# Optimization experiments

Measured on AMD Instinct MI355X. Metric: run time of the kernel, lower is better.

Reference implementation:

```python
import jax, jax.numpy as jnp
import numpy as np
from jax import lax

RADII = (0.1, 0.2, 0.4)
NBRS = (16, 32, 64)
PE_DIM = 24
CENTER_PE_DIM = 96
EPS = 1e-5


def sinusoidal_3d(x, dim):
    # x: [..., 3] -> [..., dim]; dim//3 features per axis (half sin, half cos)
    per_axis = dim // 3
    half = per_axis // 2
    freq = jnp.exp(-jnp.log(10000.0) * jnp.arange(half, dtype=x.dtype) / (half - 1))
    ang = x[..., None] * freq                      # [..., 3, half]
    emb = jnp.concatenate([jnp.sin(ang), jnp.cos(ang)], axis=-1)  # [..., 3, per_axis]
    return emb.reshape(x.shape[:-1] + (dim,))


def layer_norm(x, g, b):
    m = jnp.mean(x, axis=-1, keepdims=True)
    v = jnp.var(x, axis=-1, keepdims=True)
    return (x - m) * lax.rsqrt(v + EPS) * g + b


def point_mlp(x, W, b, g, beta, act):
    y = layer_norm(x @ W + b, g, beta)
    return jax.nn.gelu(y, approximate=False) if act else y


def index_points(pts, idx):
    # pts: [B,N,C], idx: [B,...] -> [B,...,C]
    bidx = jnp.arange(pts.shape[0]).reshape((-1,) + (1,) * (idx.ndim - 1))
    return pts[bidx, idx]


def farthest_point_sample(xyz, npoint):
    # xyz: [B,N,3] -> idx [B,npoint]
    N = xyz.shape[1]

    def single(pts):
        def step(carry, _):
            dist, far = carry
            c = pts[far]                                   # [3]
            d = jnp.sum((pts - c) ** 2, axis=-1)           # [N]
            dist = jnp.minimum(dist, d)
            nxt = jnp.argmax(dist).astype(jnp.int32)
            return (dist, nxt), far
        init = (jnp.full((N,), 1e10, pts.dtype), jnp.int32(0))
        _, idxs = lax.scan(step, init, None, length=npoint)
        return idxs

    return jax.vmap(single)(xyz)


def query_ball_point(radius, k, xyz, centers):
    # xyz: [B,N,3], centers: [B,S,3] -> [B,S,k] neighbor indices
    N = xyz.shape[1]
    sqr = jnp.sum((centers[:, :, None, :] - xyz[:, None, :, :]) ** 2, axis=-1)  # [B,S,N]
    gidx = jnp.where(sqr > radius * radius, N, jnp.arange(N)[None, None, :])
    gidx = jnp.sort(gidx, axis=-1)[..., :k]
    first = gidx[..., :1]
    return jnp.where(gidx == N, first, gidx)


def setup_inputs() -> dict:
    key = jax.random.key(0)
    ks = jax.random.split(key, 8)
    B, N, STEM, TOK = 16, 4096, 128, 256
    d_in = STEM + 3 + PE_DIM          # 155
    d_tok_in = STEM + 3 * TOK + CENTER_PE_DIM  # 992
    sc = 0.02
    return {
        "xyz": jax.random.uniform(ks[0], (B, N, 3), dtype=jnp.float32),
        "point_feature": jax.random.normal(ks[1], (B, N, STEM), dtype=jnp.float32) * 0.1,
        "sW1": jax.random.normal(ks[2], (3, d_in, TOK), dtype=jnp.float32) * sc,
        "sb1": jnp.zeros((3, TOK)), "sg1": jnp.ones((3, TOK)), "sbeta1": jnp.zeros((3, TOK)),
        "sW2": jax.random.normal(ks[3], (3, TOK, TOK), dtype=jnp.float32) * sc,
        "sb2": jnp.zeros((3, TOK)), "sg2": jnp.ones((3, TOK)), "sbeta2": jnp.zeros((3, TOK)),
        "tW1": jax.random.normal(ks[4], (d_tok_in, TOK), dtype=jnp.float32) * sc,
        "tb1": jnp.zeros((TOK,)), "tg1": jnp.ones((TOK,)), "tbeta1": jnp.zeros((TOK,)),
        "tW2": jax.random.normal(ks[5], (TOK, TOK), dtype=jnp.float32) * sc,
        "tb2": jnp.zeros((TOK,)), "tg2": jnp.ones((TOK,)), "tbeta2": jnp.zeros((TOK,)),
    }


def reference(xyz, point_feature, sW1, sb1, sg1, sbeta1, sW2, sb2, sg2, sbeta2,
              tW1, tb1, tg1, tbeta1, tW2, tb2, tg2, tbeta2):
    S = 512  # num_patches
    center_idx = farthest_point_sample(xyz, S)            # [B,S]
    patch_center = index_points(xyz, center_idx)          # [B,S,3]
    center_feature = index_points(point_feature, center_idx)  # [B,S,STEM]

    scale_feats = []
    for s, (r, k) in enumerate(zip(RADII, NBRS)):
        nidx = query_ball_point(r, k, xyz, patch_center)  # [B,S,k]
        gxyz = index_points(xyz, nidx)                    # [B,S,k,3]
        gfeat = index_points(point_feature, nidx)         # [B,S,k,STEM]
        rel = gxyz - patch_center[:, :, None, :]
        rel_pe = sinusoidal_3d(rel, PE_DIM)
        gin = jnp.concatenate([gfeat, rel, rel_pe], axis=-1)   # [B,S,k,155]
        h = point_mlp(gin, sW1[s], sb1[s], sg1[s], sbeta1[s], True)
        h = point_mlp(h, sW2[s], sb2[s], sg2[s], sbeta2[s], False)
        scale_feats.append(jnp.max(h, axis=2))            # [B,S,TOK]

    center_pe = sinusoidal_3d(patch_center, CENTER_PE_DIM)    # [B,S,96]
    tok_in = jnp.concatenate([center_feature] + scale_feats + [center_pe], axis=-1)
    tok = point_mlp(tok_in, tW1, tb1, tg1, tbeta1, True)
    tok = point_mlp(tok, tW2, tb2, tg2, tbeta2, False)
    return tok, patch_center
```

## Files before the change

kernel.cpp:

```cpp
#include <hip/hip_runtime.h>
#include <math.h>

#define BATCH 16
#define NPTS  4096
#define NCTR  512
#define STEM  128
#define TOK   256
#define D_IN  155
#define D_TOK 992

typedef short s16x8 __attribute__((ext_vector_type(8)));
typedef float f32x4 __attribute__((ext_vector_type(4)));

static constexpr float FR15c[16] = {
    1.0f, 0.5411695265464638f, 0.2928644487857941f, 0.15848931670188904f,
    0.08576958626508713f, 0.04641588851809502f, 0.02511886507272720f, 0.01359356392547488f,
    0.007356422487646341f, 0.003981071710586548f, 0.002154434798285365f, 0.001165914465673268f,
    0.0006309573450125754f, 0.0003414548910222948f, 0.0001847849769866168f, 0.0001f};

__device__ __forceinline__ unsigned short f2bf(float f) {
    unsigned u = __float_as_uint(f);
    u += 0x7FFF + ((u >> 16) & 1);
    return (unsigned short)(u >> 16);
}
__device__ __forceinline__ float bf2f(unsigned short b) {
    return __uint_as_float(((unsigned)b) << 16);
}

__device__ __forceinline__ void bsplit8(const float* v, s16x8& hi, s16x8& lo) {
    union { s16x8 s; unsigned w[4]; } H, L;
#pragma unroll
    for (int p = 0; p < 4; ++p) {
        unsigned hp, lp;
        asm("v_cvt_pk_bf16_f32 %0, %1, %2" : "=v"(hp) : "v"(v[2 * p]), "v"(v[2 * p + 1]));
        float r0 = v[2 * p]     - __uint_as_float(hp << 16);
        float r1 = v[2 * p + 1] - __uint_as_float(hp & 0xffff0000u);
        asm("v_cvt_pk_bf16_f32 %0, %1, %2" : "=v"(lp) : "v"(r0), "v"(r1));
        H.w[p] = hp; L.w[p] = lp;
    }
    hi = H.s; lo = L.s;
}

__device__ __forceinline__ void pkpair(float v0, float v1, unsigned& w0, unsigned& w1) {
    unsigned hp, lp;
    asm("v_cvt_pk_bf16_f32 %0, %1, %2" : "=v"(hp) : "v"(v0), "v"(v1));
    float r0 = v0 - __uint_as_float(hp << 16);
    float r1 = v1 - __uint_as_float(hp & 0xffff0000u);
    asm("v_cvt_pk_bf16_f32 %0, %1, %2" : "=v"(lp) : "v"(r0), "v"(r1));
    w0 = (hp << 16) | (lp & 0xffffu);
    w1 = (hp & 0xffff0000u) | (lp >> 16);
}

__device__ __forceinline__ void loadB(const unsigned short* __restrict__ pk,
                                      int frag, int l, s16x8& bh, s16x8& bl) {
    const unsigned short* p = pk + (size_t)frag * 1024 + (size_t)l * 8;
    bh = *(const s16x8*)p;
    bl = *(const s16x8*)(p + 512);
}

__device__ __forceinline__ float gelu_exact(float x) {
    float z = x * 0.70710678118654752f;
    float a = fabsf(z);
    float t = __builtin_amdgcn_rcpf(fmaf(0.3275911f, a, 1.0f));
    float p = fmaf(1.061405429f, t, -1.453152027f);
    p = fmaf(p, t, 1.421413741f);
    p = fmaf(p, t, -0.284496736f);
    p = fmaf(p, t, 0.254829592f);
    p = p * t;
    float e = __expf(-z * z);
    float y = fmaf(-p, e, 1.0f);
    y = (z < 0.0f) ? -y : y;
    return 0.5f * x * (1.0f + y);
}

__device__ __forceinline__ float sq3(float ax, float ay, float az,
                                     float bx, float by, float bz) {
    float dx = __fsub_rn(ax, bx);
    float dy = __fsub_rn(ay, by);
    float dz = __fsub_rn(az, bz);
    float d = __fmul_rn(dx, dx);
    d = __fadd_rn(d, __fmul_rn(dy, dy));
    d = __fadd_rn(d, __fmul_rn(dz, dz));
    return d;
}

__global__ __launch_bounds__(256) void fps_kernel(const float* __restrict__ xyz,
                                                  int* __restrict__ center_idx,
                                                  float* __restrict__ pc_ws,
                                                  float* __restrict__ pc_out) {
    int b = blockIdx.x;
    int t = threadIdx.x;
    const int w = t >> 6, lane = t & 63;
    const float* X = xyz + (size_t)b * NPTS * 3;
    __shared__ __align__(16) float sxyz[NPTS * 3];
    __shared__ float swv[2][4];
    __shared__ int   swi[2][4];
    __shared__ int   hist[NCTR];
    {
        const float4* src = (const float4*)X;
        float4* dst = (float4*)sxyz;
        for (int i = t; i < NPTS * 3 / 4; i += 256) dst[i] = src[i];
    }
    __syncthreads();
    float px[16], py[16], pz[16], dist[16];
#pragma unroll
    for (int j = 0; j < 16; ++j) {
        int i = t + 256 * j;
        px[j] = sxyz[i * 3 + 0];
        py[j] = sxyz[i * 3 + 1];
        pz[j] = sxyz[i * 3 + 2];
        dist[j] = 1e10f;
    }
    int far = 0;
    for (int s = 0; s < NCTR; ++s) {
        if (t == 0) hist[s] = far;
        float cx = sxyz[far * 3 + 0];
        float cy = sxyz[far * 3 + 1];
        float cz = sxyz[far * 3 + 2];
        float bv = -1.0f;
        int bi = 0;
#pragma unroll
        for (int j = 0; j < 16; ++j) {
            float d = sq3(px[j], py[j], pz[j], cx, cy, cz);
            float nd = fminf(dist[j], d);
            dist[j] = nd;
            if (nd > bv) { bv = nd; bi = t + 256 * j; }
        }
#pragma unroll
        for (int off = 32; off >= 1; off >>= 1) {
            float ov = __shfl_xor(bv, off, 64);
            int   oi = __shfl_xor(bi, off, 64);
            if (ov > bv || (ov == bv && oi < bi)) { bv = ov; bi = oi; }
        }
        const int p = s & 1;
        if (lane == 0) { swv[p][w] = bv; swi[p][w] = bi; }
        __syncthreads();
        bv = swv[p][0]; bi = swi[p][0];
#pragma unroll
        for (int ww = 1; ww < 4; ++ww) {
            float ov = swv[p][ww]; int oi = swi[p][ww];
            if (ov > bv || (ov == bv && oi < bi)) { bv = ov; bi = oi; }
        }
        far = bi;
    }
    __syncthreads();
    for (int s = t; s < NCTR; s += 256) {
        int idx = hist[s];
        center_idx[b * NCTR + s] = idx;
        float cx = sxyz[idx * 3], cy = sxyz[idx * 3 + 1], cz = sxyz[idx * 3 + 2];
        size_t po = (size_t)(b * NCTR + s) * 3;
        pc_ws[po] = cx; pc_ws[po + 1] = cy; pc_ws[po + 2] = cz;
        pc_out[po] = cx; pc_out[po + 1] = cy; pc_out[po + 2] = cz;
    }
}

template <int K>
__global__ __launch_bounds__(256) void ballq_kernel(const float* __restrict__ xyz,
                                                    const float* __restrict__ pc,
                                                    int* __restrict__ nbr,
                                                    float rr) {
    int cid = blockIdx.x * 4 + (threadIdx.x >> 6);
    int lane = threadIdx.x & 63;
    int b = cid >> 9;
    const float* X = xyz + (size_t)b * NPTS * 3;
    float cx = pc[(size_t)cid * 3 + 0];
    float cy = pc[(size_t)cid * 3 + 1];
    float cz = pc[(size_t)cid * 3 + 2];
    int cnt = 0, first = 0;
    bool have_first = false;
    long long base = (long long)cid * K;
    for (int it = 0; it < NPTS / 64; ++it) {
        int i = it * 64 + lane;
        float d = sq3(cx, cy, cz, X[i * 3], X[i * 3 + 1], X[i * 3 + 2]);
        bool ok = d <= rr;
        unsigned long long mask = __ballot(ok);
        if (!have_first && mask) {
            first = it * 64 + (int)__builtin_ctzll(mask);
            have_first = true;
        }
        int pos = cnt + (int)__popcll(mask & ((1ull << lane) - 1ull));
        if (ok && pos < K) nbr[base + pos] = i;
        cnt += (int)__popcll(mask);
        if (cnt >= K) break;
    }
    int fill = cnt < K ? cnt : K;
    for (int j = fill + lane; j < K; j += 64) nbr[base + j] = first;
}

__global__ __launch_bounds__(256) void pack_w(const float* __restrict__ Wbase,
                                              unsigned short* __restrict__ out,
                                              int Kdim, int KS) {
    int s = blockIdx.y;
    const float* W = Wbase + (size_t)s * Kdim * TOK;
    unsigned short* o = out + (size_t)s * 16 * KS * 64 * 16;
    int tid = blockIdx.x * 256 + threadIdx.x;
    if (tid >= 16 * KS * 64) return;
    int lane = tid & 63;
    int frag = tid >> 6;
    int ks = frag % KS;
    int ct = frag / KS;
    int col = ct * 16 + (lane & 15);
    int k0 = ks * 32 + (lane >> 4) * 8;
    unsigned short* hi = o + (size_t)frag * 1024 + lane * 8;
    unsigned short* lo = hi + 512;
#pragma unroll
    for (int j = 0; j < 8; ++j) {
        int k = k0 + j;
        float v = (k < Kdim) ? W[(size_t)k * TOK + col] : 0.0f;
        unsigned short h = f2bf(v);
        hi[j] = h;
        lo[j] = f2bf(v - bf2f(h));
    }
}

template <int K>
__global__ __launch_bounds__(256, 2) void scale_mfma(
    const float* __restrict__ xyz, const float* __restrict__ pf,
    const unsigned short* __restrict__ pk1, const float* __restrict__ b1,
    const float* __restrict__ g1, const float* __restrict__ be1,
    const unsigned short* __restrict__ pk2, const float* __restrict__ b2,
    const float* __restrict__ g2, const float* __restrict__ be2,
    const int* __restrict__ nbr, const float* __restrict__ pc,
    float* __restrict__ outf) {
    __shared__ unsigned int hpk[64][260];
    __shared__ float lnred[4][64][2];
    const int w = threadIdx.x >> 6, l = threadIdx.x & 63;
    const int lg = l >> 4, li = l & 15;
    const int ws4 = 4 * w;

    int nb[4];
    float relx[4], rely[4], relz[4];
#pragma unroll
    for (int rb = 0; rb < 4; ++rb) {
        int row_g = blockIdx.x * 64 + rb * 16 + li;
        int c = (blockIdx.x * 64 + rb * 16) / K;
        int b = c >> 9;
        int n = nbr[row_g];
        nb[rb] = b * NPTS + n;
        const float* X = xyz + (size_t)nb[rb] * 3;
        const float* C = pc + (size_t)c * 3;
        relx[rb] = __fsub_rn(X[0], C[0]);
        rely[rb] = __fsub_rn(X[1], C[1]);
        relz[rb] = __fsub_rn(X[2], C[2]);
    }

    f32x4 acc1[4][4];
#pragma unroll
    for (int rb = 0; rb < 4; ++rb)
#pragma unroll
        for (int ctl = 0; ctl < 4; ++ctl) acc1[rb][ctl] = (f32x4){0.f, 0.f, 0.f, 0.f};

#pragma unroll
    for (int ks = 0; ks < 5; ++ks) {
        s16x8 Bh[4], Bl[4];
#pragma unroll
        for (int ctl = 0; ctl < 4; ++ctl)
            loadB(pk1, (ws4 + ctl) * 5 + ks, l, Bh[ctl], Bl[ctl]);
        s16x8 Ah[4], Al[4];
#pragma unroll
        for (int rb = 0; rb < 4; ++rb) {
            float v[8];
            if (ks < 4) {
                const float* src = pf + (size_t)nb[rb] * STEM + ks * 32 + lg * 8;
                float4 f0 = *(const float4*)src;
                float4 f1 = *(const float4*)(src + 4);
                v[0] = f0.x; v[1] = f0.y; v[2] = f0.z; v[3] = f0.w;
                v[4] = f1.x; v[5] = f1.y; v[6] = f1.z; v[7] = f1.w;
            } else {
#pragma unroll
                for (int j = 0; j < 8; ++j) {
                    int ch = lg * 8 + j;
                    float val = 0.0f;
                    if (ch < 3) {
                        val = (ch == 0) ? relx[rb] : ((ch == 1) ? rely[rb] : relz[rb]);
                    } else if (ch < 27) {
                        int rem = ch - 3;
                        int axis = rem >> 3, r8 = rem & 7;
                        int fi = (r8 < 4) ? r8 : r8 - 4;
                        float fr = (fi == 0) ? 1.0f
                                  : (fi == 1) ? 0.046415888336127795f
                                  : (fi == 2) ? 0.0021544346900318843f : 1e-4f;
                        float rl = (axis == 0) ? relx[rb] : ((axis == 1) ? rely[rb] : relz[rb]);
                        float ang = rl * fr;
                        val = (r8 < 4) ? __sinf(ang) : __cosf(ang);
                    }
                    v[j] = val;
                }
            }
            bsplit8(v, Ah[rb], Al[rb]);
        }
#pragma unroll
        for (int ctl = 0; ctl < 4; ++ctl)
#pragma unroll
            for (int rb = 0; rb < 4; ++rb) {
                acc1[rb][ctl] = __builtin_amdgcn_mfma_f32_16x16x32_bf16(Ah[rb], Bh[ctl], acc1[rb][ctl], 0, 0, 0);
                acc1[rb][ctl] = __builtin_amdgcn_mfma_f32_16x16x32_bf16(Ah[rb], Bl[ctl], acc1[rb][ctl], 0, 0, 0);
                acc1[rb][ctl] = __builtin_amdgcn_mfma_f32_16x16x32_bf16(Al[rb], Bh[ctl], acc1[rb][ctl], 0, 0, 0);
            }
    }

    {
        float b1v[4], g1v[4], be1v[4];
#pragma unroll
        for (int ctl = 0; ctl < 4; ++ctl) {
            int col = w * 64 + ctl * 16 + li;
            b1v[ctl] = b1[col]; g1v[ctl] = g1[col]; be1v[ctl] = be1[col];
        }
#pragma unroll
        for (int rb = 0; rb < 4; ++rb)
#pragma unroll
            for (int reg = 0; reg < 4; ++reg) {
                float s = 0.f, ss = 0.f;
#pragma unroll
                for (int ctl = 0; ctl < 4; ++ctl) {
                    float x = acc1[rb][ctl][reg] + b1v[ctl];
                    s += x; ss = fmaf(x, x, ss);
                }
#pragma unroll
                for (int m = 1; m <= 8; m <<= 1) {
                    s += __shfl_xor(s, m, 64);
                    ss += __shfl_xor(ss, m, 64);
                }
                if (li == 0) {
                    lnred[w][rb * 16 + lg * 4 + reg][0] = s;
                    lnred[w][rb * 16 + lg * 4 + reg][1] = ss;
                }
            }
        __syncthreads();
#pragma unroll
        for (int rb = 0; rb < 4; ++rb)
#pragma unroll
            for (int reg = 0; reg < 4; ++reg) {
                int row = rb * 16 + lg * 4 + reg;
                float s = lnred[0][row][0] + lnred[1][row][0] + lnred[2][row][0] + lnred[3][row][0];
                float ss = lnred[0][row][1] + lnred[1][row][1] + lnred[2][row][1] + lnred[3][row][1];
                float mean = s * (1.0f / 256.0f);
                float var = ss * (1.0f / 256.0f) - mean * mean;
                float rs = rsqrtf(var + 1e-5f);
#pragma unroll
                for (int ctl = 0; ctl < 4; ++ctl) {
                    float x = acc1[rb][ctl][reg] + b1v[ctl];
                    acc1[rb][ctl][reg] = gelu_exact((x - mean) * rs * g1v[ctl] + be1v[ctl]);
                }
            }
    }

#pragma unroll
    for (int rb = 0; rb < 4; ++rb)
#pragma unroll
        for (int ctl = 0; ctl < 4; ++ctl) {
            unsigned w0, w1, w2, w3;
            pkpair(acc1[rb][ctl][0], acc1[rb][ctl][1], w0, w1);
            pkpair(acc1[rb][ctl][2], acc1[rb][ctl][3], w2, w3);
            int r0 = rb * 16 + lg * 4;
            int kc = w * 64 + ctl * 16 + li;
            hpk[r0 + 0][kc] = w0; hpk[r0 + 1][kc] = w1;
            hpk[r0 + 2][kc] = w2; hpk[r0 + 3][kc] = w3;
        }
    __syncthreads();

    f32x4 acc2[4][4];
#pragma unroll
    for (int rb = 0; rb < 4; ++rb)
#pragma unroll
        for (int ctl = 0; ctl < 4; ++ctl) acc2[rb][ctl] = (f32x4){0.f, 0.f, 0.f, 0.f};

#pragma unroll
    for (int q = 0; q < 8; ++q) {
        s16x8 Bh[4], Bl[4];
#pragma unroll
        for (int ctl = 0; ctl < 4; ++ctl)
            loadB(pk2, (ws4 + ctl) * 8 + q, l, Bh[ctl], Bl[ctl]);
#pragma unroll
        for (int rb = 0; rb < 4; ++rb) {
            const unsigned int* hp = &hpk[rb * 16 + li][q * 32 + lg * 8];
            int4 xa = *(const int4*)hp;
            int4 xb = *(const int4*)(hp + 4);
            unsigned x[8] = {(unsigned)xa.x, (unsigned)xa.y, (unsigned)xa.z, (unsigned)xa.w,
                             (unsigned)xb.x, (unsigned)xb.y, (unsigned)xb.z, (unsigned)xb.w};
            union { s16x8 s; unsigned w[4]; } H, L;
#pragma unroll
            for (int p = 0; p < 4; ++p) {
                H.w[p] = (x[2 * p] >> 16) | (x[2 * p + 1] & 0xffff0000u);
                L.w[p] = (x[2 * p] & 0xffffu) | (x[2 * p + 1] << 16);
            }
#pragma unroll
            for (int ctl = 0; ctl < 4; ++ctl) {
                acc2[rb][ctl] = __builtin_amdgcn_mfma_f32_16x16x32_bf16(H.s, Bh[ctl], acc2[rb][ctl], 0, 0, 0);
                acc2[rb][ctl] = __builtin_amdgcn_mfma_f32_16x16x32_bf16(H.s, Bl[ctl], acc2[rb][ctl], 0, 0, 0);
                acc2[rb][ctl] = __builtin_amdgcn_mfma_f32_16x16x32_bf16(L.s, Bh[ctl], acc2[rb][ctl], 0, 0, 0);
            }
        }
    }

    float b2v[4], g2v[4], be2v[4];
#pragma unroll
    for (int ctl = 0; ctl < 4; ++ctl) {
        int col = w * 64 + ctl * 16 + li;
        b2v[ctl] = b2[col]; g2v[ctl] = g2[col]; be2v[ctl] = be2[col];
    }
#pragma unroll
    for (int rb = 0; rb < 4; ++rb)
#pragma unroll
        for (int reg = 0; reg < 4; ++reg) {
            float s = 0.f, ss = 0.f;
#pragma unroll
            for (int ctl = 0; ctl < 4; ++ctl) {
                float x = acc2[rb][ctl][reg] + b2v[ctl];
                s += x; ss = fmaf(x, x, ss);
            }
#pragma unroll
            for (int m = 1; m <= 8; m <<= 1) {
                s += __shfl_xor(s, m, 64);
                ss += __shfl_xor(ss, m, 64);
            }
            if (li == 0) {
                lnred[w][rb * 16 + lg * 4 + reg][0] = s;
                lnred[w][rb * 16 + lg * 4 + reg][1] = ss;
            }
        }
    __syncthreads();
#pragma unroll
    for (int rb = 0; rb < 4; ++rb)
#pragma unroll
        for (int reg = 0; reg < 4; ++reg) {
            int row = rb * 16 + lg * 4 + reg;
            float s = lnred[0][row][0] + lnred[1][row][0] + lnred[2][row][0] + lnred[3][row][0];
            float ss = lnred[0][row][1] + lnred[1][row][1] + lnred[2][row][1] + lnred[3][row][1];
            float mean = s * (1.0f / 256.0f);
            float var = ss * (1.0f / 256.0f) - mean * mean;
            float rs = rsqrtf(var + 1e-5f);
#pragma unroll
            for (int ctl = 0; ctl < 4; ++ctl) {
                float x = acc2[rb][ctl][reg] + b2v[ctl];
                acc2[rb][ctl][reg] = (x - mean) * rs * g2v[ctl] + be2v[ctl];
            }
        }

    const int CPB = 64 / K;
    const int RBC = K / 16;
#pragma unroll
    for (int cg = 0; cg < CPB; ++cg)
#pragma unroll
        for (int ctl = 0; ctl < 4; ++ctl) {
            float mx = -3.4e38f;
#pragma unroll
            for (int rbl = 0; rbl < RBC; ++rbl) {
                int rb = cg * RBC + rbl;
#pragma unroll
                for (int reg = 0; reg < 4; ++reg) mx = fmaxf(mx, acc2[rb][ctl][reg]);
            }
            mx = fmaxf(mx, __shfl_xor(mx, 16, 64));
            mx = fmaxf(mx, __shfl_xor(mx, 32, 64));
            if (lg == 0)
                outf[(size_t)(blockIdx.x * CPB + cg) * TOK + w * 64 + ctl * 16 + li] = mx;
        }
}

__global__ __launch_bounds__(256, 2) void token_mfma(
    const float* __restrict__ pf, const int* __restrict__ center_idx,
    const float* __restrict__ pc, const float* __restrict__ sf0,
    const float* __restrict__ sf1, const float* __restrict__ sf2,
    const unsigned short* __restrict__ pk1, const float* __restrict__ b1,
    const float* __restrict__ g1, const float* __restrict__ be1,
    const unsigned short* __restrict__ pk2, const float* __restrict__ b2,
    const float* __restrict__ g2, const float* __restrict__ be2,
    float* __restrict__ out) {
    __shared__ unsigned int hpk[32][260];
    __shared__ float lnred[4][32][2];
    const int w = threadIdx.x >> 6, l = threadIdx.x & 63;
    const int lg = l >> 4, li = l & 15;
    const int ws4 = 4 * w;
    const int rowbase = blockIdx.x * 32;

    int rowg[2];
    const float* pfc[2];
    float pcx[2], pcy[2], pcz[2];
#pragma unroll
    for (int rb = 0; rb < 2; ++rb) {
        int row = rowbase + rb * 16 + li;
        rowg[rb] = row;
        int b = row >> 9;
        int cidx = center_idx[row];
        pfc[rb] = pf + ((size_t)b * NPTS + cidx) * STEM;
        pcx[rb] = pc[(size_t)row * 3 + 0];
        pcy[rb] = pc[(size_t)row * 3 + 1];
        pcz[rb] = pc[(size_t)row * 3 + 2];
    }

    f32x4 acc1[2][4];
#pragma unroll
    for (int rb = 0; rb < 2; ++rb)
#pragma unroll
        for (int ctl = 0; ctl < 4; ++ctl) acc1[rb][ctl] = (f32x4){0.f, 0.f, 0.f, 0.f};

#pragma unroll 2
    for (int ks = 0; ks < 31; ++ks) {
        s16x8 Bh[4], Bl[4];
#pragma unroll
        for (int ctl = 0; ctl < 4; ++ctl)
            loadB(pk1, (ws4 + ctl) * 31 + ks, l, Bh[ctl], Bl[ctl]);
        s16x8 Ah[2], Al[2];
#pragma unroll
        for (int rb = 0; rb < 2; ++rb) {
            float v[8];
            if (ks < 28) {
                const float* src;
                if (ks < 4)       src = pfc[rb] + ks * 32 + lg * 8;
                else if (ks < 12) src = sf0 + (size_t)rowg[rb] * TOK + (ks - 4) * 32 + lg * 8;
                else if (ks < 20) src = sf1 + (size_t)rowg[rb] * TOK + (ks - 12) * 32 + lg * 8;
                else              src = sf2 + (size_t)rowg[rb] * TOK + (ks - 20) * 32 + lg * 8;
                float4 f0 = *(const float4*)src;
                float4 f1 = *(const float4*)(src + 4);
                v[0] = f0.x; v[1] = f0.y; v[2] = f0.z; v[3] = f0.w;
                v[4] = f1.x; v[5] = f1.y; v[6] = f1.z; v[7] = f1.w;
            } else {
                float c = (ks == 28) ? pcx[rb] : ((ks == 29) ? pcy[rb] : pcz[rb]);
#pragma unroll
                for (int j = 0; j < 8; ++j) {
                    float fr = (lg & 1) ? FR15c[8 + j] : FR15c[j];
                    float ang = c * fr;
                    v[j] = (lg < 2) ? __sinf(ang) : __cosf(ang);
                }
            }
            bsplit8(v, Ah[rb], Al[rb]);
        }
#pragma unroll
        for (int ctl = 0; ctl < 4; ++ctl)
#pragma unroll
            for (int rb = 0; rb < 2; ++rb) {
                acc1[rb][ctl] = __builtin_amdgcn_mfma_f32_16x16x32_bf16(Ah[rb], Bh[ctl], acc1[rb][ctl], 0, 0, 0);
                acc1[rb][ctl] = __builtin_amdgcn_mfma_f32_16x16x32_bf16(Ah[rb], Bl[ctl], acc1[rb][ctl], 0, 0, 0);
                acc1[rb][ctl] = __builtin_amdgcn_mfma_f32_16x16x32_bf16(Al[rb], Bh[ctl], acc1[rb][ctl], 0, 0, 0);
            }
    }

    {
        float b1v[4], g1v[4], be1v[4];
#pragma unroll
        for (int ctl = 0; ctl < 4; ++ctl) {
            int col = w * 64 + ctl * 16 + li;
            b1v[ctl] = b1[col]; g1v[ctl] = g1[col]; be1v[ctl] = be1[col];
        }
#pragma unroll
        for (int rb = 0; rb < 2; ++rb)
#pragma unroll
            for (int reg = 0; reg < 4; ++reg) {
                float s = 0.f, ss = 0.f;
#pragma unroll
                for (int ctl = 0; ctl < 4; ++ctl) {
                    float x = acc1[rb][ctl][reg] + b1v[ctl];
                    s += x; ss = fmaf(x, x, ss);
                }
#pragma unroll
                for (int m = 1; m <= 8; m <<= 1) {
                    s += __shfl_xor(s, m, 64);
                    ss += __shfl_xor(ss, m, 64);
                }
                if (li == 0) {
                    lnred[w][rb * 16 + lg * 4 + reg][0] = s;
                    lnred[w][rb * 16 + lg * 4 + reg][1] = ss;
                }
            }
        __syncthreads();
#pragma unroll
        for (int rb = 0; rb < 2; ++rb)
#pragma unroll
            for (int reg = 0; reg < 4; ++reg) {
                int row = rb * 16 + lg * 4 + reg;
                float s = lnred[0][row][0] + lnred[1][row][0] + lnred[2][row][0] + lnred[3][row][0];
                float ss = lnred[0][row][1] + lnred[1][row][1] + lnred[2][row][1] + lnred[3][row][1];
                float mean = s * (1.0f / 256.0f);
                float var = ss * (1.0f / 256.0f) - mean * mean;
                float rs = rsqrtf(var + 1e-5f);
#pragma unroll
                for (int ctl = 0; ctl < 4; ++ctl) {
                    float x = acc1[rb][ctl][reg] + b1v[ctl];
                    acc1[rb][ctl][reg] = gelu_exact((x - mean) * rs * g1v[ctl] + be1v[ctl]);
                }
            }
    }

#pragma unroll
    for (int rb = 0; rb < 2; ++rb)
#pragma unroll
        for (int ctl = 0; ctl < 4; ++ctl) {
            unsigned w0, w1, w2, w3;
            pkpair(acc1[rb][ctl][0], acc1[rb][ctl][1], w0, w1);
            pkpair(acc1[rb][ctl][2], acc1[rb][ctl][3], w2, w3);
            int r0 = rb * 16 + lg * 4;
            int kc = w * 64 + ctl * 16 + li;
            hpk[r0 + 0][kc] = w0; hpk[r0 + 1][kc] = w1;
            hpk[r0 + 2][kc] = w2; hpk[r0 + 3][kc] = w3;
        }
    __syncthreads();

    f32x4 acc2[2][4];
#pragma unroll
    for (int rb = 0; rb < 2; ++rb)
#pragma unroll
        for (int ctl = 0; ctl < 4; ++ctl) acc2[rb][ctl] = (f32x4){0.f, 0.f, 0.f, 0.f};
#pragma unroll
    for (int q = 0; q < 8; ++q) {
        s16x8 Bh[4], Bl[4];
#pragma unroll
        for (int ctl = 0; ctl < 4; ++ctl)
            loadB(pk2, (ws4 + ctl) * 8 + q, l, Bh[ctl], Bl[ctl]);
#pragma unroll
        for (int rb = 0; rb < 2; ++rb) {
            const unsigned int* hp = &hpk[rb * 16 + li][q * 32 + lg * 8];
            int4 xa = *(const int4*)hp;
            int4 xb = *(const int4*)(hp + 4);
            unsigned x[8] = {(unsigned)xa.x, (unsigned)xa.y, (unsigned)xa.z, (unsigned)xa.w,
                             (unsigned)xb.x, (unsigned)xb.y, (unsigned)xb.z, (unsigned)xb.w};
            union { s16x8 s; unsigned w[4]; } H, L;
#pragma unroll
            for (int p = 0; p < 4; ++p) {
                H.w[p] = (x[2 * p] >> 16) | (x[2 * p + 1] & 0xffff0000u);
                L.w[p] = (x[2 * p] & 0xffffu) | (x[2 * p + 1] << 16);
            }
#pragma unroll
            for (int ctl = 0; ctl < 4; ++ctl) {
                acc2[rb][ctl] = __builtin_amdgcn_mfma_f32_16x16x32_bf16(H.s, Bh[ctl], acc2[rb][ctl], 0, 0, 0);
                acc2[rb][ctl] = __builtin_amdgcn_mfma_f32_16x16x32_bf16(H.s, Bl[ctl], acc2[rb][ctl], 0, 0, 0);
                acc2[rb][ctl] = __builtin_amdgcn_mfma_f32_16x16x32_bf16(L.s, Bh[ctl], acc2[rb][ctl], 0, 0, 0);
            }
        }
    }

    float b2v[4], g2v[4], be2v[4];
#pragma unroll
    for (int ctl = 0; ctl < 4; ++ctl) {
        int col = w * 64 + ctl * 16 + li;
        b2v[ctl] = b2[col]; g2v[ctl] = g2[col]; be2v[ctl] = be2[col];
    }
#pragma unroll
    for (int rb = 0; rb < 2; ++rb)
#pragma unroll
        for (int reg = 0; reg < 4; ++reg) {
            float s = 0.f, ss = 0.f;
#pragma unroll
            for (int ctl = 0; ctl < 4; ++ctl) {
                float x = acc2[rb][ctl][reg] + b2v[ctl];
                s += x; ss = fmaf(x, x, ss);
            }
#pragma unroll
            for (int m = 1; m <= 8; m <<= 1) {
                s += __shfl_xor(s, m, 64);
                ss += __shfl_xor(ss, m, 64);
            }
            if (li == 0) {
                lnred[w][rb * 16 + lg * 4 + reg][0] = s;
                lnred[w][rb * 16 + lg * 4 + reg][1] = ss;
            }
        }
    __syncthreads();
#pragma unroll
    for (int rb = 0; rb < 2; ++rb)
#pragma unroll
        for (int reg = 0; reg < 4; ++reg) {
            int row = rb * 16 + lg * 4 + reg;
            float s = lnred[0][row][0] + lnred[1][row][0] + lnred[2][row][0] + lnred[3][row][0];
            float ss = lnred[0][row][1] + lnred[1][row][1] + lnred[2][row][1] + lnred[3][row][1];
            float mean = s * (1.0f / 256.0f);
            float var = ss * (1.0f / 256.0f) - mean * mean;
            float rs = rsqrtf(var + 1e-5f);
#pragma unroll
            for (int ctl = 0; ctl < 4; ++ctl) {
                float x = acc2[rb][ctl][reg] + b2v[ctl];
                float v = (x - mean) * rs * g2v[ctl] + be2v[ctl];
                out[(size_t)(rowbase + row) * TOK + w * 64 + ctl * 16 + li] = v;
            }
        }
}

extern "C" void kernel_launch(void* const* d_in, const int* in_sizes, int n_in,
                              void* d_out, int out_size, void* d_ws, size_t ws_size,
                              hipStream_t stream) {
    const float* xyz  = (const float*)d_in[0];
    const float* pf   = (const float*)d_in[1];
    const float* sW1  = (const float*)d_in[2];
    const float* sb1  = (const float*)d_in[3];
    const float* sg1  = (const float*)d_in[4];
    const float* sbe1 = (const float*)d_in[5];
    const float* sW2  = (const float*)d_in[6];
    const float* sb2  = (const float*)d_in[7];
    const float* sg2  = (const float*)d_in[8];
    const float* sbe2 = (const float*)d_in[9];
    const float* tW1  = (const float*)d_in[10];
    const float* tb1  = (const float*)d_in[11];
    const float* tg1  = (const float*)d_in[12];
    const float* tbe1 = (const float*)d_in[13];
    const float* tW2  = (const float*)d_in[14];
    const float* tb2  = (const float*)d_in[15];
    const float* tg2  = (const float*)d_in[16];
    const float* tbe2 = (const float*)d_in[17];

    float* out_tok = (float*)d_out;
    float* out_pc  = out_tok + (size_t)BATCH * NCTR * TOK;

    char* ws = (char*)d_ws;
    int* center_idx = (int*)ws;   ws += (size_t)BATCH * NCTR * 4;
    float* pc_ws    = (float*)ws; ws += (size_t)BATCH * NCTR * 3 * 4;
    int* nbr0       = (int*)ws;   ws += (size_t)BATCH * NCTR * 16 * 4;
    int* nbr1       = (int*)ws;   ws += (size_t)BATCH * NCTR * 32 * 4;
    int* nbr2       = (int*)ws;   ws += (size_t)BATCH * NCTR * 64 * 4;
    float* sf0      = (float*)ws; ws += (size_t)BATCH * NCTR * TOK * 4;
    float* sf1      = (float*)ws; ws += (size_t)BATCH * NCTR * TOK * 4;
    float* sf2      = (float*)ws; ws += (size_t)BATCH * NCTR * TOK * 4;
    const size_t PK1_S  = 16 * 5 * 64 * 16;
    const size_t PK2_S  = 16 * 8 * 64 * 16;
    const size_t PKT1_S = 16 * 31 * 64 * 16;
    const size_t PKT2_S = 16 * 8 * 64 * 16;
    unsigned short* pkW1 = (unsigned short*)ws; ws += 3 * PK1_S * 2;
    unsigned short* pkW2 = (unsigned short*)ws; ws += 3 * PK2_S * 2;
    unsigned short* pkT1 = (unsigned short*)ws; ws += PKT1_S * 2;
    unsigned short* pkT2 = (unsigned short*)ws; ws += PKT2_S * 2;

    {
        dim3 gp1((16 * 5 * 64 + 255) / 256, 3);
        pack_w<<<gp1, 256, 0, stream>>>(sW1, pkW1, D_IN, 5);
        dim3 gp2((16 * 8 * 64 + 255) / 256, 3);
        pack_w<<<gp2, 256, 0, stream>>>(sW2, pkW2, TOK, 8);
        dim3 gpt1((16 * 31 * 64 + 255) / 256, 1);
        pack_w<<<gpt1, 256, 0, stream>>>(tW1, pkT1, D_TOK, 31);
        dim3 gpt2((16 * 8 * 64 + 255) / 256, 1);
        pack_w<<<gpt2, 256, 0, stream>>>(tW2, pkT2, TOK, 8);
    }

    fps_kernel<<<BATCH, 256, 0, stream>>>(xyz, center_idx, pc_ws, out_pc);

    ballq_kernel<16><<<BATCH * NCTR / 4, 256, 0, stream>>>(xyz, pc_ws, nbr0, (float)(0.1 * 0.1));
    ballq_kernel<32><<<BATCH * NCTR / 4, 256, 0, stream>>>(xyz, pc_ws, nbr1, (float)(0.2 * 0.2));
    ballq_kernel<64><<<BATCH * NCTR / 4, 256, 0, stream>>>(xyz, pc_ws, nbr2, (float)(0.4 * 0.4));

    scale_mfma<16><<<(BATCH * NCTR * 16) / 64, 256, 0, stream>>>(
        xyz, pf, pkW1 + 0 * PK1_S, sb1 + 0 * TOK, sg1 + 0 * TOK, sbe1 + 0 * TOK,
        pkW2 + 0 * PK2_S, sb2 + 0 * TOK, sg2 + 0 * TOK, sbe2 + 0 * TOK,
        nbr0, pc_ws, sf0);
    scale_mfma<32><<<(BATCH * NCTR * 32) / 64, 256, 0, stream>>>(
        xyz, pf, pkW1 + 1 * PK1_S, sb1 + 1 * TOK, sg1 + 1 * TOK, sbe1 + 1 * TOK,
        pkW2 + 1 * PK2_S, sb2 + 1 * TOK, sg2 + 1 * TOK, sbe2 + 1 * TOK,
        nbr1, pc_ws, sf1);
    scale_mfma<64><<<(BATCH * NCTR * 64) / 64, 256, 0, stream>>>(
        xyz, pf, pkW1 + 2 * PK1_S, sb1 + 2 * TOK, sg1 + 2 * TOK, sbe1 + 2 * TOK,
        pkW2 + 2 * PK2_S, sb2 + 2 * TOK, sg2 + 2 * TOK, sbe2 + 2 * TOK,
        nbr2, pc_ws, sf2);

    token_mfma<<<(BATCH * NCTR) / 32, 256, 0, stream>>>(
        pf, center_idx, pc_ws, sf0, sf1, sf2,
        pkT1, tb1, tg1, tbe1, pkT2, tb2, tg2, tbe2, out_tok);
}
```

Baseline: 1.634 ms.

## Halve scale MLP block tile to 32 rows and defer K=64 max to token kernel

Each scale_mfma block now handles 32 neighbor rows instead of 64, which halves accumulator registers and LDS use and doubles the grid. This is meant to raise occupancy or cut register pressure and spills. With K=64 a center now spans two blocks, so those blocks write partial maxima to a doubled buffer. token_mfma takes the max of the two partials while loading its input. The cost is more blocks, more reloads of the packed weights, and extra global traffic for the K=64 partials.

```diff
diff --git a/kernel.cpp b/kernel.cpp
--- a/kernel.cpp
+++ b/kernel.cpp
@@ -222,18 +222,18 @@
     const float* __restrict__ g2, const float* __restrict__ be2,
     const int* __restrict__ nbr, const float* __restrict__ pc,
     float* __restrict__ outf) {
-    __shared__ unsigned int hpk[64][260];
-    __shared__ float lnred[4][64][2];
+    __shared__ unsigned int hpk[32][260];
+    __shared__ float lnred[4][32][2];
     const int w = threadIdx.x >> 6, l = threadIdx.x & 63;
     const int lg = l >> 4, li = l & 15;
     const int ws4 = 4 * w;
 
-    int nb[4];
-    float relx[4], rely[4], relz[4];
-#pragma unroll
-    for (int rb = 0; rb < 4; ++rb) {
-        int row_g = blockIdx.x * 64 + rb * 16 + li;
-        int c = (blockIdx.x * 64 + rb * 16) / K;
+    int nb[2];
+    float relx[2], rely[2], relz[2];
+#pragma unroll
+    for (int rb = 0; rb < 2; ++rb) {
+        int row_g = blockIdx.x * 32 + rb * 16 + li;
+        int c = (blockIdx.x * 32 + rb * 16) / K;
         int b = c >> 9;
         int n = nbr[row_g];
         nb[rb] = b * NPTS + n;
@@ -244,9 +244,9 @@
         relz[rb] = __fsub_rn(X[2], C[2]);
     }
 
-    f32x4 acc1[4][4];
-#pragma unroll
-    for (int rb = 0; rb < 4; ++rb)
+    f32x4 acc1[2][4];
+#pragma unroll
+    for (int rb = 0; rb < 2; ++rb)
 #pragma unroll
         for (int ctl = 0; ctl < 4; ++ctl) acc1[rb][ctl] = (f32x4){0.f, 0.f, 0.f, 0.f};
 
@@ -256,9 +256,9 @@
 #pragma unroll
         for (int ctl = 0; ctl < 4; ++ctl)
             loadB(pk1, (ws4 + ctl) * 5 + ks, l, Bh[ctl], Bl[ctl]);
-        s16x8 Ah[4], Al[4];
-#pragma unroll
-        for (int rb = 0; rb < 4; ++rb) {
+        s16x8 Ah[2], Al[2];
+#pragma unroll
+        for (int rb = 0; rb < 2; ++rb) {
             float v[8];
             if (ks < 4) {
                 const float* src = pf + (size_t)nb[rb] * STEM + ks * 32 + lg * 8;
@@ -292,7 +292,7 @@
 #pragma unroll
         for (int ctl = 0; ctl < 4; ++ctl)
 #pragma unroll
-            for (int rb = 0; rb < 4; ++rb) {
+            for (int rb = 0; rb < 2; ++rb) {
                 acc1[rb][ctl] = __builtin_amdgcn_mfma_f32_16x16x32_bf16(Ah[rb], Bh[ctl], acc1[rb][ctl], 0, 0, 0);
                 acc1[rb][ctl] = __builtin_amdgcn_mfma_f32_16x16x32_bf16(Ah[rb], Bl[ctl], acc1[rb][ctl], 0, 0, 0);
                 acc1[rb][ctl] = __builtin_amdgcn_mfma_f32_16x16x32_bf16(Al[rb], Bh[ctl], acc1[rb][ctl], 0, 0, 0);
@@ -307,7 +307,7 @@
             b1v[ctl] = b1[col]; g1v[ctl] = g1[col]; be1v[ctl] = be1[col];
         }
 #pragma unroll
-        for (int rb = 0; rb < 4; ++rb)
+        for (int rb = 0; rb < 2; ++rb)
 #pragma unroll
             for (int reg = 0; reg < 4; ++reg) {
                 float s = 0.f, ss = 0.f;
@@ -328,7 +328,7 @@
             }
         __syncthreads();
 #pragma unroll
-        for (int rb = 0; rb < 4; ++rb)
+        for (int rb = 0; rb < 2; ++rb)
 #pragma unroll
             for (int reg = 0; reg < 4; ++reg) {
                 int row = rb * 16 + lg * 4 + reg;
@@ -346,7 +346,7 @@
     }
 
 #pragma unroll
-    for (int rb = 0; rb < 4; ++rb)
+    for (int rb = 0; rb < 2; ++rb)
 #pragma unroll
         for (int ctl = 0; ctl < 4; ++ctl) {
             unsigned w0, w1, w2, w3;
@@ -359,9 +359,9 @@
         }
     __syncthreads();
 
-    f32x4 acc2[4][4];
-#pragma unroll
-    for (int rb = 0; rb < 4; ++rb)
+    f32x4 acc2[2][4];
+#pragma unroll
+    for (int rb = 0; rb < 2; ++rb)
 #pragma unroll
         for (int ctl = 0; ctl < 4; ++ctl) acc2[rb][ctl] = (f32x4){0.f, 0.f, 0.f, 0.f};
 
@@ -372,7 +372,7 @@
         for (int ctl = 0; ctl < 4; ++ctl)
             loadB(pk2, (ws4 + ctl) * 8 + q, l, Bh[ctl], Bl[ctl]);
 #pragma unroll
-        for (int rb = 0; rb < 4; ++rb) {
+        for (int rb = 0; rb < 2; ++rb) {
             const unsigned int* hp = &hpk[rb * 16 + li][q * 32 + lg * 8];
             int4 xa = *(const int4*)hp;
             int4 xb = *(const int4*)(hp + 4);
@@ -400,7 +400,7 @@
         b2v[ctl] = b2[col]; g2v[ctl] = g2[col]; be2v[ctl] = be2[col];
     }
 #pragma unroll
-    for (int rb = 0; rb < 4; ++rb)
+    for (int rb = 0; rb < 2; ++rb)
 #pragma unroll
         for (int reg = 0; reg < 4; ++reg) {
             float s = 0.f, ss = 0.f;
@@ -421,7 +421,7 @@
         }
     __syncthreads();
 #pragma unroll
-    for (int rb = 0; rb < 4; ++rb)
+    for (int rb = 0; rb < 2; ++rb)
 #pragma unroll
         for (int reg = 0; reg < 4; ++reg) {
             int row = rb * 16 + lg * 4 + reg;
@@ -437,30 +437,39 @@
             }
         }
 
-    const int CPB = 64 / K;
-    const int RBC = K / 16;
-#pragma unroll
-    for (int cg = 0; cg < CPB; ++cg)
+    if (K == 16) {
+#pragma unroll
+        for (int rb = 0; rb < 2; ++rb)
+#pragma unroll
+            for (int ctl = 0; ctl < 4; ++ctl) {
+                float mx = -3.4e38f;
+#pragma unroll
+                for (int reg = 0; reg < 4; ++reg) mx = fmaxf(mx, acc2[rb][ctl][reg]);
+                mx = fmaxf(mx, __shfl_xor(mx, 16, 64));
+                mx = fmaxf(mx, __shfl_xor(mx, 32, 64));
+                if (lg == 0)
+                    outf[(size_t)(blockIdx.x * 2 + rb) * TOK + w * 64 + ctl * 16 + li] = mx;
+            }
+    } else {
 #pragma unroll
         for (int ctl = 0; ctl < 4; ++ctl) {
             float mx = -3.4e38f;
 #pragma unroll
-            for (int rbl = 0; rbl < RBC; ++rbl) {
-                int rb = cg * RBC + rbl;
+            for (int rb = 0; rb < 2; ++rb)
 #pragma unroll
                 for (int reg = 0; reg < 4; ++reg) mx = fmaxf(mx, acc2[rb][ctl][reg]);
-            }
             mx = fmaxf(mx, __shfl_xor(mx, 16, 64));
             mx = fmaxf(mx, __shfl_xor(mx, 32, 64));
             if (lg == 0)
-                outf[(size_t)(blockIdx.x * CPB + cg) * TOK + w * 64 + ctl * 16 + li] = mx;
-        }
+                outf[(size_t)blockIdx.x * TOK + w * 64 + ctl * 16 + li] = mx;
+        }
+    }
 }
 
 __global__ __launch_bounds__(256, 2) void token_mfma(
     const float* __restrict__ pf, const int* __restrict__ center_idx,
     const float* __restrict__ pc, const float* __restrict__ sf0,
-    const float* __restrict__ sf1, const float* __restrict__ sf2,
+    const float* __restrict__ sf1, const float* __restrict__ sf2p,
     const unsigned short* __restrict__ pk1, const float* __restrict__ b1,
     const float* __restrict__ g1, const float* __restrict__ be1,
     const unsigned short* __restrict__ pk2, const float* __restrict__ b2,
@@ -504,16 +513,26 @@
 #pragma unroll
         for (int rb = 0; rb < 2; ++rb) {
             float v[8];
-            if (ks < 28) {
+            if (ks < 20) {
                 const float* src;
                 if (ks < 4)       src = pfc[rb] + ks * 32 + lg * 8;
                 else if (ks < 12) src = sf0 + (size_t)rowg[rb] * TOK + (ks - 4) * 32 + lg * 8;
-                else if (ks < 20) src = sf1 + (size_t)rowg[rb] * TOK + (ks - 12) * 32 + lg * 8;
-                else              src = sf2 + (size_t)rowg[rb] * TOK + (ks - 20) * 32 + lg * 8;
+                else              src = sf1 + (size_t)rowg[rb] * TOK + (ks - 12) * 32 + lg * 8;
                 float4 f0 = *(const float4*)src;
                 float4 f1 = *(const float4*)(src + 4);
                 v[0] = f0.x; v[1] = f0.y; v[2] = f0.z; v[3] = f0.w;
                 v[4] = f1.x; v[5] = f1.y; v[6] = f1.z; v[7] = f1.w;
+            } else if (ks < 28) {
+                const float* sa = sf2p + ((size_t)rowg[rb] * 2) * TOK + (ks - 20) * 32 + lg * 8;
+                const float* sb = sa + TOK;
+                float4 a0 = *(const float4*)sa;
+                float4 a1 = *(const float4*)(sa + 4);
+                float4 b0 = *(const float4*)sb;
+                float4 b1 = *(const float4*)(sb + 4);
+                v[0] = fmaxf(a0.x, b0.x); v[1] = fmaxf(a0.y, b0.y);
+                v[2] = fmaxf(a0.z, b0.z); v[3] = fmaxf(a0.w, b0.w);
+                v[4] = fmaxf(a1.x, b1.x); v[5] = fmaxf(a1.y, b1.y);
+                v[6] = fmaxf(a1.z, b1.z); v[7] = fmaxf(a1.w, b1.w);
             } else {
                 float c = (ks == 28) ? pcx[rb] : ((ks == 29) ? pcy[rb] : pcz[rb]);
 #pragma unroll
@@ -707,7 +726,7 @@
     int* nbr2       = (int*)ws;   ws += (size_t)BATCH * NCTR * 64 * 4;
     float* sf0      = (float*)ws; ws += (size_t)BATCH * NCTR * TOK * 4;
     float* sf1      = (float*)ws; ws += (size_t)BATCH * NCTR * TOK * 4;
-    float* sf2      = (float*)ws; ws += (size_t)BATCH * NCTR * TOK * 4;
+    float* sf2p     = (float*)ws; ws += (size_t)BATCH * NCTR * 2 * TOK * 4;
     const size_t PK1_S  = 16 * 5 * 64 * 16;
     const size_t PK2_S  = 16 * 8 * 64 * 16;
     const size_t PKT1_S = 16 * 31 * 64 * 16;
@@ -734,20 +753,20 @@
     ballq_kernel<32><<<BATCH * NCTR / 4, 256, 0, stream>>>(xyz, pc_ws, nbr1, (float)(0.2 * 0.2));
     ballq_kernel<64><<<BATCH * NCTR / 4, 256, 0, stream>>>(xyz, pc_ws, nbr2, (float)(0.4 * 0.4));
 
-    scale_mfma<16><<<(BATCH * NCTR * 16) / 64, 256, 0, stream>>>(
+    scale_mfma<16><<<(BATCH * NCTR * 16) / 32, 256, 0, stream>>>(
         xyz, pf, pkW1 + 0 * PK1_S, sb1 + 0 * TOK, sg1 + 0 * TOK, sbe1 + 0 * TOK,
         pkW2 + 0 * PK2_S, sb2 + 0 * TOK, sg2 + 0 * TOK, sbe2 + 0 * TOK,
         nbr0, pc_ws, sf0);
-    scale_mfma<32><<<(BATCH * NCTR * 32) / 64, 256, 0, stream>>>(
+    scale_mfma<32><<<(BATCH * NCTR * 32) / 32, 256, 0, stream>>>(
         xyz, pf, pkW1 + 1 * PK1_S, sb1 + 1 * TOK, sg1 + 1 * TOK, sbe1 + 1 * TOK,
         pkW2 + 1 * PK2_S, sb2 + 1 * TOK, sg2 + 1 * TOK, sbe2 + 1 * TOK,
         nbr1, pc_ws, sf1);
-    scale_mfma<64><<<(BATCH * NCTR * 64) / 64, 256, 0, stream>>>(
+    scale_mfma<64><<<(BATCH * NCTR * 64) / 32, 256, 0, stream>>>(
         xyz, pf, pkW1 + 2 * PK1_S, sb1 + 2 * TOK, sg1 + 2 * TOK, sbe1 + 2 * TOK,
         pkW2 + 2 * PK2_S, sb2 + 2 * TOK, sg2 + 2 * TOK, sbe2 + 2 * TOK,
-        nbr2, pc_ws, sf2);
+        nbr2, pc_ws, sf2p);
 
     token_mfma<<<(BATCH * NCTR) / 32, 256, 0, stream>>>(
-        pf, center_idx, pc_ws, sf0, sf1, sf2,
+        pf, center_idx, pc_ws, sf0, sf1, sf2p,
         pkT1, tb1, tg1, tbe1, pkT2, tb2, tg2, tbe2, out_tok);
 }
```

After: 1.590 ms. -2.7%, faster.
